# Performance work log

Hardware: AMD Instinct MI355X
Metric: run time of the kernel (lower is better)

The kernel has to match this reference:

```python
import jax, jax.numpy as jnp
import numpy as np

N_NODES = 50000
N_EDGES = 500000
IN_CH = 256
HID = 64
HEADS = 8
OUT_CH = 16
NEG_SLOPE = 0.2  # PyG GATConv default


def setup_inputs() -> dict:
    key = jax.random.key(0)
    ks = jax.random.split(key, 10)
    x = jax.random.normal(ks[0], (N_NODES, IN_CH), dtype=jnp.float32)
    edge_index = jax.random.randint(ks[1], (2, N_EDGES), 0, N_NODES, dtype=jnp.int64)
    s1 = 1.0 / np.sqrt(IN_CH)
    W1 = jax.random.uniform(ks[2], (IN_CH, HEADS * HID), jnp.float32, -s1, s1)
    att_src1 = jax.random.normal(ks[3], (HEADS, HID), dtype=jnp.float32) * 0.1
    att_dst1 = jax.random.normal(ks[4], (HEADS, HID), dtype=jnp.float32) * 0.1
    b1 = jnp.zeros((HEADS * HID,), jnp.float32)
    s2 = 1.0 / np.sqrt(HEADS * HID)
    W2 = jax.random.uniform(ks[5], (HEADS * HID, OUT_CH), jnp.float32, -s2, s2)
    att_src2 = jax.random.normal(ks[6], (1, OUT_CH), dtype=jnp.float32) * 0.1
    att_dst2 = jax.random.normal(ks[7], (1, OUT_CH), dtype=jnp.float32) * 0.1
    b2 = jnp.zeros((OUT_CH,), jnp.float32)
    return {"x": x, "edge_index": edge_index, "W1": W1, "att_src1": att_src1,
            "att_dst1": att_dst1, "b1": b1, "W2": W2, "att_src2": att_src2,
            "att_dst2": att_dst2, "b2": b2}


def _gat_conv(x, src, dst, W, att_src, att_dst, bias, heads, out_ch, concat, n_nodes):
    # Linear transform: [N, H, C]
    h = (x @ W).reshape(n_nodes, heads, out_ch)
    # Per-node attention logits: [N, H]
    a_src = jnp.einsum('nhc,hc->nh', h, att_src)
    a_dst = jnp.einsum('nhc,hc->nh', h, att_dst)
    # Edge-wise attention score (message src -> dst): [E, H]
    e = jax.nn.leaky_relu(a_src[src] + a_dst[dst], NEG_SLOPE)
    # Segment softmax over incoming edges of each destination node
    emax = jax.ops.segment_max(e, dst, num_segments=n_nodes)  # [N, H]
    emax = jnp.where(jnp.isfinite(emax), emax, 0.0)
    e = jnp.exp(e - emax[dst])
    denom = jax.ops.segment_sum(e, dst, num_segments=n_nodes)  # [N, H]
    alpha = e / (denom[dst] + 1e-16)
    # Weighted scatter-add aggregation: [N, H, C]
    msg = h[src] * alpha[:, :, None]
    out = jax.ops.segment_sum(msg, dst, num_segments=n_nodes)
    if concat:
        out = out.reshape(n_nodes, heads * out_ch)
    else:
        out = out.mean(axis=1)
    return out + bias


def reference(x, edge_index, W1, att_src1, att_dst1, b1, W2, att_src2, att_dst2, b2):
    n = x.shape[0]
    # PyG GATConv adds self-loops by default
    loops = jnp.arange(n, dtype=edge_index.dtype)
    src = jnp.concatenate([edge_index[0], loops])
    dst = jnp.concatenate([edge_index[1], loops])
    # dropout (p=0.6) is identity in eval mode
    h = _gat_conv(x, src, dst, W1, att_src1, att_dst1, b1, HEADS, HID, True, n)
    h = jax.nn.elu(h)
    out = _gat_conv(h, src, dst, W2, att_src2, att_dst2, b2, 1, OUT_CH, False, n)
    return jax.nn.log_softmax(out, axis=1)
```

## Files before the change

### kernel.cpp

```cpp
#include <hip/hip_runtime.h>
#include <math.h>

#define N_NODES 50000
#define N_EDGES 500000
#define IN_CH 256
#define D1 512
#define HEADS 8
#define HID 64
#define OUT_CH 16
#define NEG_SLOPE 0.2f

typedef __bf16 bf16x8 __attribute__((ext_vector_type(8)));
typedef float f32x4 __attribute__((ext_vector_type(4)));
typedef float f32x2 __attribute__((ext_vector_type(2)));

__device__ inline void fp8x8_to_f32(uint2 u, float* f) {
    f32x2 p0 = __builtin_amdgcn_cvt_pk_f32_fp8(u.x, false);
    f32x2 p1 = __builtin_amdgcn_cvt_pk_f32_fp8(u.x, true);
    f32x2 p2 = __builtin_amdgcn_cvt_pk_f32_fp8(u.y, false);
    f32x2 p3 = __builtin_amdgcn_cvt_pk_f32_fp8(u.y, true);
    f[0] = p0.x; f[1] = p0.y; f[2] = p1.x; f[3] = p1.y;
    f[4] = p2.x; f[5] = p2.y; f[6] = p3.x; f[7] = p3.y;
}

__device__ inline void fp8x16_to_f32(uint4 u, float* f) {
    fp8x8_to_f32(make_uint2(u.x, u.y), f);
    fp8x8_to_f32(make_uint2(u.z, u.w), f + 8);
}

__device__ inline unsigned char f32_to_fp8(float v) {
    return (unsigned char)(__builtin_amdgcn_cvt_pk_fp8_f32(v, v, 0, false) & 0xff);
}

__device__ inline void gl_lds16(const __bf16* g, __bf16* l) {
    __builtin_amdgcn_global_load_lds(
        (const __attribute__((address_space(1))) unsigned int*)g,
        (__attribute__((address_space(3))) unsigned int*)l,
        16, 0, 0);
}

__global__ __launch_bounds__(256) void k_prep(const float* __restrict__ X,
                                              const float* __restrict__ W1,
                                              const float* __restrict__ W2,
                                              const int* __restrict__ edst,
                                              __bf16* __restrict__ Xb,
                                              __bf16* __restrict__ Wt,
                                              __bf16* __restrict__ Wt2,
                                              int* __restrict__ deg) {
    int t = blockIdx.x * 256 + threadIdx.x;
    int nthr = gridDim.x * 256;
    for (int i = t; i < N_NODES * IN_CH / 8; i += nthr) {
        size_t base = (size_t)i * 8;
        float4 v0 = *(const float4*)&X[base];
        float4 v1 = *(const float4*)&X[base + 4];
        __bf16 o[8] = {(__bf16)v0.x, (__bf16)v0.y, (__bf16)v0.z, (__bf16)v0.w,
                       (__bf16)v1.x, (__bf16)v1.y, (__bf16)v1.z, (__bf16)v1.w};
        *(uint4*)&Xb[base] = *(uint4*)o;
    }
    for (int i = t; i < D1 * IN_CH; i += nthr) {
        int n = i >> 8, k = i & 255;
        Wt[i] = (__bf16)W1[k * D1 + n];
    }
    for (int i = t; i < D1 * OUT_CH; i += nthr) {
        int n = i >> 9, k = i & 511;
        Wt2[i] = (__bf16)W2[k * OUT_CH + n];
    }
    for (int i = t; i < N_EDGES; i += nthr) atomicAdd(&deg[edst[i]], 1);
}

__global__ __launch_bounds__(256) void k_gemm1_mfma(const __bf16* __restrict__ Xb,
                                                    const __bf16* __restrict__ Wt,
                                                    const float* __restrict__ att_src,
                                                    const float* __restrict__ att_dst,
                                                    unsigned char* __restrict__ Hf8,
                                                    float* __restrict__ a_src1,
                                                    float* __restrict__ a_dst1) {
    __shared__ __align__(16) __bf16 As[128 * 64];
    __shared__ __align__(16) __bf16 Bs[128 * 64];
    int tid = threadIdx.x;
    int wid = tid >> 6, lane = tid & 63;
    int wr = wid >> 1, wc = wid & 1;
    int row0 = blockIdx.x * 128;
    int col0 = blockIdx.y * 128;
    int lq = lane >> 4;
    int lm = lane & 15;
    int sw = lm & 7;
    int r_st[4], g_st[4];
    #pragma unroll
    for (int it = 0; it < 4; ++it) {
        int idx = tid + it * 256;
        int r = idx >> 3;
        int p = idx & 7;
        r_st[it] = r;
        g_st[it] = (p ^ (r & 7)) * 8;
    }
    f32x4 acc[4][4] = {};
    for (int kt = 0; kt < IN_CH / 64; ++kt) {
        int k0 = kt * 64;
        #pragma unroll
        for (int it = 0; it < 4; ++it) {
            int idx = tid + it * 256;
            gl_lds16(&Xb[(size_t)(row0 + r_st[it]) * IN_CH + k0 + g_st[it]], &As[idx * 8]);
            gl_lds16(&Wt[(size_t)(col0 + r_st[it]) * IN_CH + k0 + g_st[it]], &Bs[idx * 8]);
        }
        __syncthreads();
        #pragma unroll
        for (int kt2 = 0; kt2 < 2; ++kt2) {
            bf16x8 af[4], bfr[4];
            #pragma unroll
            for (int i = 0; i < 4; ++i)
                af[i]  = *(bf16x8*)&As[(wr * 64 + i * 16 + lm) * 64 + (((kt2 * 4 + lq) ^ sw) * 8)];
            #pragma unroll
            for (int j = 0; j < 4; ++j)
                bfr[j] = *(bf16x8*)&Bs[(wc * 64 + j * 16 + lm) * 64 + (((kt2 * 4 + lq) ^ sw) * 8)];
            #pragma unroll
            for (int i = 0; i < 4; ++i)
                #pragma unroll
                for (int j = 0; j < 4; ++j)
                    acc[i][j] = __builtin_amdgcn_mfma_f32_16x16x32_bf16(af[i], bfr[j], acc[i][j], 0, 0, 0);
        }
        __syncthreads();
    }
    int head = blockIdx.y * 2 + wc;
    float as_v[4], ad_v[4];
    #pragma unroll
    for (int j = 0; j < 4; ++j) {
        as_v[j] = att_src[head * HID + j * 16 + lm];
        ad_v[j] = att_dst[head * HID + j * 16 + lm];
    }
    #pragma unroll
    for (int i = 0; i < 4; ++i) {
        int rbase = row0 + wr * 64 + i * 16 + lq * 4;
        #pragma unroll
        for (int r = 0; r < 4; ++r) {
            int grow = rbase + r;
            float ps = 0.f, pd = 0.f;
            #pragma unroll
            for (int j = 0; j < 4; ++j) {
                float v = acc[i][j][r];
                ps += v * as_v[j];
                pd += v * ad_v[j];
                if (grow < N_NODES)
                    Hf8[(size_t)grow * D1 + col0 + wc * 64 + j * 16 + lm] = f32_to_fp8(v);
            }
            #pragma unroll
            for (int off = 1; off < 16; off <<= 1) {
                ps += __shfl_xor(ps, off);
                pd += __shfl_xor(pd, off);
            }
            if (lm == 0 && grow < N_NODES) {
                a_src1[grow * HEADS + head] = ps;
                a_dst1[grow * HEADS + head] = pd;
            }
        }
    }
}

__global__ __launch_bounds__(1024) void k_scan1(const int* __restrict__ deg,
                                                int* __restrict__ offsets,
                                                int* __restrict__ bsum) {
    __shared__ int wsum[16];
    int tid = threadIdx.x, lane = tid & 63, wid = tid >> 6;
    int i = blockIdx.x * 1024 + tid;
    int v = (i < N_NODES) ? deg[i] : 0;
    int x = v;
    #pragma unroll
    for (int off = 1; off < 64; off <<= 1) {
        int t = __shfl_up(x, off);
        if (lane >= off) x += t;
    }
    if (lane == 63) wsum[wid] = x;
    __syncthreads();
    if (wid == 0) {
        int s = (lane < 16) ? wsum[lane] : 0;
        #pragma unroll
        for (int off = 1; off < 16; off <<= 1) {
            int t = __shfl_up(s, off);
            if (lane >= off) s += t;
        }
        if (lane < 16) wsum[lane] = s;
    }
    __syncthreads();
    int wbase = wid ? wsum[wid - 1] : 0;
    if (i < N_NODES) offsets[i] = wbase + x - v;
    if (tid == 1023) bsum[blockIdx.x] = wsum[15];
}

__global__ __launch_bounds__(256) void k_scan3(int* __restrict__ offsets,
                                               const int* __restrict__ bsum,
                                               int* __restrict__ cursor) {
    __shared__ int bpre_s[64];
    int tid = threadIdx.x;
    const int nb = (N_NODES + 1023) / 1024;
    if (tid < 64) {
        int v = (tid < nb) ? bsum[tid] : 0;
        int x = v;
        #pragma unroll
        for (int off = 1; off < 64; off <<= 1) {
            int t = __shfl_up(x, off);
            if (tid >= off) x += t;
        }
        bpre_s[tid] = x - v;
        if (blockIdx.x == 0 && tid == nb - 1) offsets[N_NODES] = x;
    }
    __syncthreads();
    int i = blockIdx.x * 256 + tid;
    if (i < N_NODES) {
        int o = offsets[i] + bpre_s[i >> 10];
        offsets[i] = o;
        cursor[i] = o;
    }
}

__global__ void k_scatter(const int* __restrict__ esrc, const int* __restrict__ edst,
                          const float* __restrict__ a_src, const float* __restrict__ a_dst,
                          int* __restrict__ cursor, int* __restrict__ csr,
                          float* __restrict__ w1) {
    int e = blockIdx.x * blockDim.x + threadIdx.x;
    if (e >= N_EDGES) return;
    int s = esrc[e], d = edst[e];
    int pos = atomicAdd(&cursor[d], 1);
    csr[pos] = s;
    float4 s0 = *(const float4*)&a_src[s * HEADS];
    float4 s1 = *(const float4*)&a_src[s * HEADS + 4];
    float4 d0 = *(const float4*)&a_dst[d * HEADS];
    float4 d1 = *(const float4*)&a_dst[d * HEADS + 4];
    float ev[8] = {s0.x + d0.x, s0.y + d0.y, s0.z + d0.z, s0.w + d0.w,
                   s1.x + d1.x, s1.y + d1.y, s1.z + d1.z, s1.w + d1.w};
    float w[8];
    #pragma unroll
    for (int h = 0; h < 8; ++h) {
        float v = ev[h] > 0.f ? ev[h] : NEG_SLOPE * ev[h];
        w[h] = __expf(v);
    }
    *(float4*)&w1[(size_t)pos * 8]     = make_float4(w[0], w[1], w[2], w[3]);
    *(float4*)&w1[(size_t)pos * 8 + 4] = make_float4(w[4], w[5], w[6], w[7]);
}

__global__ __launch_bounds__(256) void k_agg1(const unsigned char* __restrict__ Hf8,
                                              const float* __restrict__ a_src,
                                              const float* __restrict__ a_dst,
                                              const float* __restrict__ w1,
                                              const int* __restrict__ offsets,
                                              const int* __restrict__ csr,
                                              const float* __restrict__ b1,
                                              __bf16* __restrict__ OUT) {
    int wave = (blockIdx.x * blockDim.x + threadIdx.x) >> 6;
    int lane = threadIdx.x & 63;
    if (wave >= N_NODES) return;
    int d = wave;
    int half = lane >> 5;
    int l32 = lane & 31;
    int chb = l32 * 16;
    int head = l32 >> 2;
    float o[16];
    #pragma unroll
    for (int j = 0; j < 16; ++j) o[j] = 0.f;
    float lsum = 0.f;
    if (half == 0) {
        float es = a_src[d * HEADS + head] + a_dst[d * HEADS + head];
        es = es > 0.f ? es : NEG_SLOPE * es;
        float wself = __expf(es);
        uint4 hu = *(const uint4*)&Hf8[(size_t)d * D1 + chb];
        float hv[16];
        fp8x16_to_f32(hu, hv);
        lsum = wself;
        #pragma unroll
        for (int j = 0; j < 16; ++j) o[j] = wself * hv[j];
    }
    int beg = offsets[d], end = offsets[d + 1];
    int idx = beg;
    for (; idx + 4 <= end; idx += 4) {
        int eA = idx + half, eB = idx + 2 + half;
        int sA = csr[eA], sB = csr[eB];
        float wA = w1[(size_t)eA * 8 + head];
        float wB = w1[(size_t)eB * 8 + head];
        uint4 uA = *(const uint4*)&Hf8[(size_t)sA * D1 + chb];
        uint4 uB = *(const uint4*)&Hf8[(size_t)sB * D1 + chb];
        float fA[16], fB[16];
        fp8x16_to_f32(uA, fA);
        fp8x16_to_f32(uB, fB);
        lsum += wA + wB;
        #pragma unroll
        for (int j = 0; j < 16; ++j) o[j] += wA * fA[j] + wB * fB[j];
    }
    for (; idx < end; idx += 2) {
        int e = idx + half;
        bool valid = e < end;
        int s = valid ? csr[e] : csr[idx];
        float w = valid ? w1[(size_t)e * 8 + head] : 0.f;
        uint4 u = *(const uint4*)&Hf8[(size_t)s * D1 + chb];
        float f[16];
        fp8x16_to_f32(u, f);
        lsum += w;
        #pragma unroll
        for (int j = 0; j < 16; ++j) o[j] += w * f[j];
    }
    #pragma unroll
    for (int j = 0; j < 16; ++j) o[j] += __shfl_xor(o[j], 32);
    lsum += __shfl_xor(lsum, 32);
    if (half == 0) {
        float inv = 1.0f / (lsum + 1e-16f);
        __bf16 r[16];
        #pragma unroll
        for (int j = 0; j < 16; ++j) {
            float v = o[j] * inv + b1[chb + j];
            v = v > 0.f ? v : (__expf(v) - 1.0f);
            r[j] = (__bf16)v;
        }
        *(uint4*)&OUT[(size_t)d * D1 + chb]     = *(uint4*)&r[0];
        *(uint4*)&OUT[(size_t)d * D1 + chb + 8] = *(uint4*)&r[8];
    }
}

__global__ __launch_bounds__(256) void k_gemm2_mfma(const __bf16* __restrict__ A,
                                                    const __bf16* __restrict__ Wt2,
                                                    const float* __restrict__ as2v,
                                                    const float* __restrict__ ad2v,
                                                    __bf16* __restrict__ H2,
                                                    float* __restrict__ a_src2,
                                                    float* __restrict__ a_dst2) {
    int tid = threadIdx.x;
    int wid = tid >> 6, lane = tid & 63;
    int lq = lane >> 4, lm = lane & 15;
    int row0 = blockIdx.x * 64 + wid * 16;
    int arow = row0 + lm;
    const __bf16* ap = A + (size_t)(arow < N_NODES ? arow : 0) * D1;
    f32x4 acc = {};
    #pragma unroll
    for (int k0 = 0; k0 < 16; ++k0) {
        bf16x8 af  = *(const bf16x8*)&ap[k0 * 32 + lq * 8];
        bf16x8 bfr = *(const bf16x8*)&Wt2[lm * D1 + k0 * 32 + lq * 8];
        acc = __builtin_amdgcn_mfma_f32_16x16x32_bf16(af, bfr, acc, 0, 0, 0);
    }
    float as_c = as2v[lm], ad_c = ad2v[lm];
    #pragma unroll
    for (int r = 0; r < 4; ++r) {
        int gr = row0 + lq * 4 + r;
        float v = acc[r];
        if (gr < N_NODES) H2[gr * OUT_CH + lm] = (__bf16)v;
        float ps = v * as_c, pd = v * ad_c;
        #pragma unroll
        for (int off = 1; off < 16; off <<= 1) {
            ps += __shfl_xor(ps, off);
            pd += __shfl_xor(pd, off);
        }
        if (lm == 0 && gr < N_NODES) { a_src2[gr] = ps; a_dst2[gr] = pd; }
    }
}

__global__ __launch_bounds__(256) void k_agg2(const __bf16* __restrict__ H2,
                                              const float* __restrict__ a_src,
                                              const float* __restrict__ a_dst,
                                              const int* __restrict__ offsets,
                                              const int* __restrict__ csr,
                                              const float* __restrict__ b2,
                                              float* __restrict__ OUT) {
    int wave = (blockIdx.x * blockDim.x + threadIdx.x) >> 6;
    int lane = threadIdx.x & 63;
    if (wave >= N_NODES) return;
    int d = wave;
    int g = lane >> 4, c = lane & 15;
    float ad = a_dst[d];
    float es = a_src[d] + ad;
    es = es > 0.f ? es : NEG_SLOPE * es;
    float wself = __expf(es);
    int beg = offsets[d], end = offsets[d + 1];
    float o = 0.f, lsum = 0.f;
    if (g == 0) {
        o = wself * (float)H2[d * OUT_CH + c];
        lsum = wself;
    }
    for (int idx = beg + g; idx < end; idx += 4) {
        int s = csr[idx];
        float e = a_src[s] + ad;
        e = e > 0.f ? e : NEG_SLOPE * e;
        float w = __expf(e);
        lsum += w;
        o += w * (float)H2[s * OUT_CH + c];
    }
    o += __shfl_xor(o, 16);  o += __shfl_xor(o, 32);
    lsum += __shfl_xor(lsum, 16);  lsum += __shfl_xor(lsum, 32);
    float v = o / (lsum + 1e-16f) + b2[c];
    float mx = v;
    #pragma unroll
    for (int off = 1; off < 16; off <<= 1) mx = fmaxf(mx, __shfl_xor(mx, off));
    float se = __expf(v - mx);
    #pragma unroll
    for (int off = 1; off < 16; off <<= 1) se += __shfl_xor(se, off);
    float res = v - mx - logf(se);
    if (lane < 16) OUT[d * OUT_CH + lane] = res;
}

extern "C" void kernel_launch(void* const* d_in, const int* in_sizes, int n_in,
                              void* d_out, int out_size, void* d_ws, size_t ws_size,
                              hipStream_t stream) {
    const float* x        = (const float*)d_in[0];
    const int*   ei       = (const int*)d_in[1];
    const float* W1       = (const float*)d_in[2];
    const float* att_src1 = (const float*)d_in[3];
    const float* att_dst1 = (const float*)d_in[4];
    const float* b1       = (const float*)d_in[5];
    const float* W2       = (const float*)d_in[6];
    const float* att_src2 = (const float*)d_in[7];
    const float* att_dst2 = (const float*)d_in[8];
    const float* b2       = (const float*)d_in[9];
    float* out = (float*)d_out;

    const int* esrc = ei;
    const int* edst = ei + N_EDGES;

    char* ws = (char*)d_ws;
    size_t off = 0;
    auto alloc = [&](size_t bytes) { char* p = ws + off; off = (off + bytes + 255) & ~(size_t)255; return p; };
    unsigned char* Hf8 = (unsigned char*)alloc((size_t)N_NODES * D1);
    __bf16* out1   = (__bf16*)alloc((size_t)N_NODES * D1 * 2);
    __bf16* Xb     = (__bf16*)alloc((size_t)N_NODES * IN_CH * 2);
    __bf16* Wt     = (__bf16*)alloc((size_t)D1 * IN_CH * 2);
    __bf16* Wt2    = (__bf16*)alloc((size_t)D1 * OUT_CH * 2);
    float* a_src1  = (float*)alloc((size_t)N_NODES * HEADS * 4);
    float* a_dst1  = (float*)alloc((size_t)N_NODES * HEADS * 4);
    float* w1      = (float*)alloc((size_t)N_EDGES * HEADS * 4);
    __bf16* h2     = (__bf16*)alloc((size_t)N_NODES * OUT_CH * 2);
    float* a_src2  = (float*)alloc((size_t)N_NODES * 4);
    float* a_dst2  = (float*)alloc((size_t)N_NODES * 4);
    int*   deg     = (int*)alloc((size_t)N_NODES * 4);
    int*   offsets = (int*)alloc((size_t)(N_NODES + 1) * 4);
    int*   cursor  = (int*)alloc((size_t)N_NODES * 4);
    int*   csr     = (int*)alloc((size_t)N_EDGES * 4);
    int*   bsum    = (int*)alloc(64 * 4);
    (void)ws_size;

    hipMemsetAsync(deg, 0, (size_t)N_NODES * 4, stream);
    k_prep<<<512, 256, 0, stream>>>(x, W1, W2, edst, Xb, Wt, Wt2, deg);
    dim3 g1((N_NODES + 127) / 128, D1 / 128);
    k_gemm1_mfma<<<g1, 256, 0, stream>>>(Xb, Wt, att_src1, att_dst1, Hf8, a_src1, a_dst1);
    int nb = (N_NODES + 1023) / 1024;
    k_scan1<<<nb, 1024, 0, stream>>>(deg, offsets, bsum);
    k_scan3<<<(N_NODES + 255) / 256, 256, 0, stream>>>(offsets, bsum, cursor);
    k_scatter<<<(N_EDGES + 255) / 256, 256, 0, stream>>>(esrc, edst, a_src1, a_dst1,
                                                         cursor, csr, w1);
    k_agg1<<<(N_NODES * 64 + 255) / 256, 256, 0, stream>>>(Hf8, a_src1, a_dst1, w1, offsets, csr, b1, out1);
    k_gemm2_mfma<<<(N_NODES + 63) / 64, 256, 0, stream>>>(out1, Wt2, att_src2, att_dst2, h2, a_src2, a_dst2);
    k_agg2<<<(N_NODES * 64 + 255) / 256, 256, 0, stream>>>(h2, a_src2, a_dst2, offsets, csr, b2, out);
}
```

Before: 302.8 us.

## Recompute edge weights in aggregation and batch CSR index loads via shuffles

Removes the per-edge weight buffer written by the scatter kernel. Layer-1 aggregation now recomputes leaky-relu/exp from a_src gathers instead of reading it. Both aggregation kernels load up to 64 CSR neighbor indices per wave in one coalesced read and broadcast them with shuffles. Layer 1 is also unrolled to four neighbors per half-wave step to raise memory-level parallelism. This saves a 16 MB write and its scattered reads, at the cost of an extra a_src gather and exp per edge per lane.

```diff
diff --git a/kernel.cpp b/kernel.cpp
--- a/kernel.cpp
+++ b/kernel.cpp
@@ -30,6 +30,11 @@
 
 __device__ inline unsigned char f32_to_fp8(float v) {
     return (unsigned char)(__builtin_amdgcn_cvt_pk_fp8_f32(v, v, 0, false) & 0xff);
+}
+
+__device__ inline float leaky_exp(float e) {
+    float v = e > 0.f ? e : NEG_SLOPE * e;
+    return __expf(v);
 }
 
 __device__ inline void gl_lds16(const __bf16* g, __bf16* l) {
@@ -213,34 +218,17 @@
 }
 
 __global__ void k_scatter(const int* __restrict__ esrc, const int* __restrict__ edst,
-                          const float* __restrict__ a_src, const float* __restrict__ a_dst,
-                          int* __restrict__ cursor, int* __restrict__ csr,
-                          float* __restrict__ w1) {
+                          int* __restrict__ cursor, int* __restrict__ csr) {
     int e = blockIdx.x * blockDim.x + threadIdx.x;
     if (e >= N_EDGES) return;
     int s = esrc[e], d = edst[e];
     int pos = atomicAdd(&cursor[d], 1);
     csr[pos] = s;
-    float4 s0 = *(const float4*)&a_src[s * HEADS];
-    float4 s1 = *(const float4*)&a_src[s * HEADS + 4];
-    float4 d0 = *(const float4*)&a_dst[d * HEADS];
-    float4 d1 = *(const float4*)&a_dst[d * HEADS + 4];
-    float ev[8] = {s0.x + d0.x, s0.y + d0.y, s0.z + d0.z, s0.w + d0.w,
-                   s1.x + d1.x, s1.y + d1.y, s1.z + d1.z, s1.w + d1.w};
-    float w[8];
-    #pragma unroll
-    for (int h = 0; h < 8; ++h) {
-        float v = ev[h] > 0.f ? ev[h] : NEG_SLOPE * ev[h];
-        w[h] = __expf(v);
-    }
-    *(float4*)&w1[(size_t)pos * 8]     = make_float4(w[0], w[1], w[2], w[3]);
-    *(float4*)&w1[(size_t)pos * 8 + 4] = make_float4(w[4], w[5], w[6], w[7]);
 }
 
 __global__ __launch_bounds__(256) void k_agg1(const unsigned char* __restrict__ Hf8,
                                               const float* __restrict__ a_src,
                                               const float* __restrict__ a_dst,
-                                              const float* __restrict__ w1,
                                               const int* __restrict__ offsets,
                                               const int* __restrict__ csr,
                                               const float* __restrict__ b1,
@@ -253,14 +241,13 @@
     int l32 = lane & 31;
     int chb = l32 * 16;
     int head = l32 >> 2;
+    float ad_h = a_dst[d * HEADS + head];
     float o[16];
     #pragma unroll
     for (int j = 0; j < 16; ++j) o[j] = 0.f;
     float lsum = 0.f;
     if (half == 0) {
-        float es = a_src[d * HEADS + head] + a_dst[d * HEADS + head];
-        es = es > 0.f ? es : NEG_SLOPE * es;
-        float wself = __expf(es);
+        float wself = leaky_exp(a_src[d * HEADS + head] + ad_h);
         uint4 hu = *(const uint4*)&Hf8[(size_t)d * D1 + chb];
         float hv[16];
         fp8x16_to_f32(hu, hv);
@@ -269,32 +256,61 @@
         for (int j = 0; j < 16; ++j) o[j] = wself * hv[j];
     }
     int beg = offsets[d], end = offsets[d + 1];
-    int idx = beg;
-    for (; idx + 4 <= end; idx += 4) {
-        int eA = idx + half, eB = idx + 2 + half;
-        int sA = csr[eA], sB = csr[eB];
-        float wA = w1[(size_t)eA * 8 + head];
-        float wB = w1[(size_t)eB * 8 + head];
-        uint4 uA = *(const uint4*)&Hf8[(size_t)sA * D1 + chb];
-        uint4 uB = *(const uint4*)&Hf8[(size_t)sB * D1 + chb];
-        float fA[16], fB[16];
-        fp8x16_to_f32(uA, fA);
-        fp8x16_to_f32(uB, fB);
-        lsum += wA + wB;
-        #pragma unroll
-        for (int j = 0; j < 16; ++j) o[j] += wA * fA[j] + wB * fB[j];
-    }
-    for (; idx < end; idx += 2) {
-        int e = idx + half;
-        bool valid = e < end;
-        int s = valid ? csr[e] : csr[idx];
-        float w = valid ? w1[(size_t)e * 8 + head] : 0.f;
-        uint4 u = *(const uint4*)&Hf8[(size_t)s * D1 + chb];
-        float f[16];
-        fp8x16_to_f32(u, f);
-        lsum += w;
-        #pragma unroll
-        for (int j = 0; j < 16; ++j) o[j] += w * f[j];
+    int deg = end - beg;
+    for (int base = 0; base < deg; base += 64) {
+        int n = deg - base; if (n > 64) n = 64;
+        int sIdx = csr[beg + base + (lane < n ? lane : n - 1)];
+        int i = 0;
+        for (; i + 8 <= n; i += 8) {
+            int s0 = __shfl(sIdx, i + half);
+            int s1 = __shfl(sIdx, i + 2 + half);
+            int s2 = __shfl(sIdx, i + 4 + half);
+            int s3 = __shfl(sIdx, i + 6 + half);
+            uint4 u0 = *(const uint4*)&Hf8[(size_t)s0 * D1 + chb];
+            uint4 u1 = *(const uint4*)&Hf8[(size_t)s1 * D1 + chb];
+            uint4 u2 = *(const uint4*)&Hf8[(size_t)s2 * D1 + chb];
+            uint4 u3 = *(const uint4*)&Hf8[(size_t)s3 * D1 + chb];
+            float wt0 = leaky_exp(a_src[s0 * HEADS + head] + ad_h);
+            float wt1 = leaky_exp(a_src[s1 * HEADS + head] + ad_h);
+            float wt2 = leaky_exp(a_src[s2 * HEADS + head] + ad_h);
+            float wt3 = leaky_exp(a_src[s3 * HEADS + head] + ad_h);
+            lsum += (wt0 + wt1) + (wt2 + wt3);
+            float f0[16], f1[16], f2[16], f3[16];
+            fp8x16_to_f32(u0, f0);
+            fp8x16_to_f32(u1, f1);
+            #pragma unroll
+            for (int j = 0; j < 16; ++j) o[j] += wt0 * f0[j] + wt1 * f1[j];
+            fp8x16_to_f32(u2, f2);
+            fp8x16_to_f32(u3, f3);
+            #pragma unroll
+            for (int j = 0; j < 16; ++j) o[j] += wt2 * f2[j] + wt3 * f3[j];
+        }
+        for (; i + 4 <= n; i += 4) {
+            int s0 = __shfl(sIdx, i + half);
+            int s1 = __shfl(sIdx, i + 2 + half);
+            uint4 u0 = *(const uint4*)&Hf8[(size_t)s0 * D1 + chb];
+            uint4 u1 = *(const uint4*)&Hf8[(size_t)s1 * D1 + chb];
+            float wt0 = leaky_exp(a_src[s0 * HEADS + head] + ad_h);
+            float wt1 = leaky_exp(a_src[s1 * HEADS + head] + ad_h);
+            lsum += wt0 + wt1;
+            float f0[16], f1[16];
+            fp8x16_to_f32(u0, f0);
+            fp8x16_to_f32(u1, f1);
+            #pragma unroll
+            for (int j = 0; j < 16; ++j) o[j] += wt0 * f0[j] + wt1 * f1[j];
+        }
+        for (; i < n; i += 2) {
+            int e = i + half;
+            bool valid = e < n;
+            int s = __shfl(sIdx, valid ? e : 0);
+            float wt = valid ? leaky_exp(a_src[s * HEADS + head] + ad_h) : 0.f;
+            uint4 u = *(const uint4*)&Hf8[(size_t)s * D1 + chb];
+            float f[16];
+            fp8x16_to_f32(u, f);
+            lsum += wt;
+            #pragma unroll
+            for (int j = 0; j < 16; ++j) o[j] += wt * f[j];
+        }
     }
     #pragma unroll
     for (int j = 0; j < 16; ++j) o[j] += __shfl_xor(o[j], 32);
@@ -362,22 +378,37 @@
     int d = wave;
     int g = lane >> 4, c = lane & 15;
     float ad = a_dst[d];
-    float es = a_src[d] + ad;
-    es = es > 0.f ? es : NEG_SLOPE * es;
-    float wself = __expf(es);
-    int beg = offsets[d], end = offsets[d + 1];
     float o = 0.f, lsum = 0.f;
     if (g == 0) {
+        float wself = leaky_exp(a_src[d] + ad);
         o = wself * (float)H2[d * OUT_CH + c];
         lsum = wself;
     }
-    for (int idx = beg + g; idx < end; idx += 4) {
-        int s = csr[idx];
-        float e = a_src[s] + ad;
-        e = e > 0.f ? e : NEG_SLOPE * e;
-        float w = __expf(e);
-        lsum += w;
-        o += w * (float)H2[s * OUT_CH + c];
+    int beg = offsets[d], end = offsets[d + 1];
+    int deg = end - beg;
+    for (int base = 0; base < deg; base += 64) {
+        int n = deg - base; if (n > 64) n = 64;
+        int sIdx = csr[beg + base + (lane < n ? lane : n - 1)];
+        int i = 0;
+        for (; i + 8 <= n; i += 8) {
+            int s0 = __shfl(sIdx, i + g);
+            int s1 = __shfl(sIdx, i + 4 + g);
+            float h0 = (float)H2[s0 * OUT_CH + c];
+            float h1 = (float)H2[s1 * OUT_CH + c];
+            float wt0 = leaky_exp(a_src[s0] + ad);
+            float wt1 = leaky_exp(a_src[s1] + ad);
+            lsum += wt0 + wt1;
+            o += wt0 * h0 + wt1 * h1;
+        }
+        for (; i < n; i += 4) {
+            int e = i + g;
+            bool valid = e < n;
+            int s = __shfl(sIdx, valid ? e : 0);
+            float wt = valid ? leaky_exp(a_src[s] + ad) : 0.f;
+            float h = (float)H2[s * OUT_CH + c];
+            lsum += wt;
+            o += wt * h;
+        }
     }
     o += __shfl_xor(o, 16);  o += __shfl_xor(o, 32);
     lsum += __shfl_xor(lsum, 16);  lsum += __shfl_xor(lsum, 32);
@@ -420,7 +451,6 @@
     __bf16* Wt2    = (__bf16*)alloc((size_t)D1 * OUT_CH * 2);
     float* a_src1  = (float*)alloc((size_t)N_NODES * HEADS * 4);
     float* a_dst1  = (float*)alloc((size_t)N_NODES * HEADS * 4);
-    float* w1      = (float*)alloc((size_t)N_EDGES * HEADS * 4);
     __bf16* h2     = (__bf16*)alloc((size_t)N_NODES * OUT_CH * 2);
     float* a_src2  = (float*)alloc((size_t)N_NODES * 4);
     float* a_dst2  = (float*)alloc((size_t)N_NODES * 4);
@@ -438,9 +468,8 @@
     int nb = (N_NODES + 1023) / 1024;
     k_scan1<<<nb, 1024, 0, stream>>>(deg, offsets, bsum);
     k_scan3<<<(N_NODES + 255) / 256, 256, 0, stream>>>(offsets, bsum, cursor);
-    k_scatter<<<(N_EDGES + 255) / 256, 256, 0, stream>>>(esrc, edst, a_src1, a_dst1,
-                                                         cursor, csr, w1);
-    k_agg1<<<(N_NODES * 64 + 255) / 256, 256, 0, stream>>>(Hf8, a_src1, a_dst1, w1, offsets, csr, b1, out1);
+    k_scatter<<<(N_EDGES + 255) / 256, 256, 0, stream>>>(esrc, edst, cursor, csr);
+    k_agg1<<<(N_NODES * 64 + 255) / 256, 256, 0, stream>>>(Hf8, a_src1, a_dst1, offsets, csr, b1, out1);
     k_gemm2_mfma<<<(N_NODES + 63) / 64, 256, 0, stream>>>(out1, Wt2, att_src2, att_dst2, h2, a_src2, a_dst2);
     k_agg2<<<(N_NODES * 64 + 255) / 256, 256, 0, stream>>>(h2, a_src2, a_dst2, offsets, csr, b2, out);
 }
```

Result: faster. 296.3 us (-2.1%).
